# Kernel tuning notes

Measured on AMD Instinct MI355X. Metric: run time of the kernel, lower is better.

The kernel has to match this reference:

```python
import jax, jax.numpy as jnp
import numpy as np
import math

B, C, H, W = 32, 128, 32, 32
NUM_HEADS = 4
GROUPS = 32
EPS = 1e-5


def setup_inputs() -> dict:
    key = jax.random.key(0)
    ks = jax.random.split(key, 6)
    x = jax.random.normal(ks[0], (B, C, H, W), jnp.float32)
    norm_w = 1.0 + 0.1 * jax.random.normal(ks[1], (C,), jnp.float32)
    norm_b = 0.1 * jax.random.normal(ks[2], (C,), jnp.float32)
    qkv_w = jax.random.normal(ks[3], (3 * C, C), jnp.float32) / math.sqrt(C)
    proj_w = jax.random.normal(ks[4], (C, C), jnp.float32) / math.sqrt(C)
    proj_b = 0.01 * jax.random.normal(ks[5], (C,), jnp.float32)
    return {"x": x, "norm_w": norm_w, "norm_b": norm_b, "qkv_w": qkv_w,
            "proj_w": proj_w, "proj_b": proj_b}


def _group_norm(x, w, b):
    b_, c, h, w_ = x.shape
    xg = x.reshape(b_, GROUPS, c // GROUPS, h, w_)
    mu = xg.mean(axis=(2, 3, 4), keepdims=True)
    var = xg.var(axis=(2, 3, 4), keepdims=True)
    xn = ((xg - mu) * jax.lax.rsqrt(var + EPS)).reshape(b_, c, h, w_)
    return xn * w[None, :, None, None] + b[None, :, None, None]


def reference(x, norm_w, norm_b, qkv_w, proj_w, proj_b):
    b, c, h, w = x.shape
    nh = NUM_HEADS
    dh = c // nh
    hw = h * w
    xn = _group_norm(x, norm_w, norm_b)
    # 1x1 conv (no bias): [B,3C,H,W] flattened to [B,3C,HW]
    qkv = jnp.einsum('oc,bchw->bohw', qkv_w, xn).reshape(b, nh, 3 * dh, hw)
    # torch reshape (B*nh, 3C/nh, HW) + chunk(3, dim=1): per-head interleave
    q, k, v = qkv[:, :, :dh], qkv[:, :, dh:2 * dh], qkv[:, :, 2 * dh:]
    scale = 1.0 / math.sqrt(dh)
    # scale applied to BOTH q and k, as in the source
    attn = jnp.einsum('bhct,bhcs->bhts', q * scale, k * scale)  # [B,nh,HW,HW]
    attn = jax.nn.softmax(attn, axis=-1)
    hout = jnp.einsum('bhts,bhcs->bhct', attn, v).reshape(b, c, h, w)
    hout = jnp.einsum('oc,bchw->bohw', proj_w, hout) + proj_b[None, :, None, None]
    return hout + x
```

## Files before the change

### kernel.cpp

```cpp
#include <hip/hip_runtime.h>
#include <math.h>

#define BB 32
#define CC 128
#define HW 1024
#define NG 32
#define TPG 4096
#define QSZ ((size_t)BB * 4 * HW * 32)

typedef __attribute__((ext_vector_type(8))) short fragAB;
typedef __attribute__((ext_vector_type(4))) float fragC;
typedef __attribute__((ext_vector_type(8))) ushort ushort8v;

__device__ __forceinline__ ushort f2bf(float f) {
  union { float f; uint u; } v; v.f = f;
  uint r = v.u + 0x7FFFu + ((v.u >> 16) & 1u);
  return (ushort)(r >> 16);
}
__device__ __forceinline__ uint pack2(float lo, float hi) {
  return __builtin_amdgcn_perm(__float_as_uint(hi), __float_as_uint(lo), 0x07060302u);
}
__device__ __forceinline__ float bflo(uint u) { return __uint_as_float(u << 16); }
__device__ __forceinline__ float bfhi(uint u) { return __uint_as_float(u & 0xffff0000u); }
__device__ __forceinline__ int vswz(int row, int g) {
  return row * 128 + 16 * (g ^ (row & 7));
}

__global__ __launch_bounds__(256) void gn_stats(const float* __restrict__ x,
    float2* __restrict__ stats, const float* __restrict__ qkvw,
    const float* __restrict__ projw, ushort* __restrict__ wq16,
    ushort* __restrict__ wp16) {
  if (blockIdx.x >= 1024) {
    int idx = (blockIdx.x - 1024) * 256 + threadIdx.x;
    if (idx < 49152) wq16[idx] = f2bf(qkvw[idx]);
    else             wp16[idx - 49152] = f2bf(projw[idx - 49152]);
    return;
  }
  int blk = blockIdx.x;
  int b = blk >> 5, g = blk & 31;
  const float4* xp4 = (const float4*)(x + ((size_t)(b * CC + g * 4)) * HW);
  float s = 0.f, s2 = 0.f;
  #pragma unroll
  for (int i = 0; i < 4; ++i) {
    float4 v = xp4[threadIdx.x + i * 256];
    s  += v.x + v.y + v.z + v.w;
    s2 += v.x * v.x + v.y * v.y + v.z * v.z + v.w * v.w;
  }
  #pragma unroll
  for (int off = 32; off; off >>= 1) {
    s  += __shfl_down(s, off, 64);
    s2 += __shfl_down(s2, off, 64);
  }
  __shared__ float ls[4], ls2[4];
  int lane = threadIdx.x & 63, wid = threadIdx.x >> 6;
  if (lane == 0) { ls[wid] = s; ls2[wid] = s2; }
  __syncthreads();
  if (threadIdx.x == 0) {
    float a  = ls[0] + ls[1] + ls[2] + ls[3];
    float a2 = ls2[0] + ls2[1] + ls2[2] + ls2[3];
    float mu = a * (1.f / TPG);
    float var = a2 * (1.f / TPG) - mu * mu;
    stats[blk] = make_float2(mu, rsqrtf(var + 1e-5f));
  }
}

template<int PROJ>
__global__ __launch_bounds__(256) void mgemm(
    const ushort* __restrict__ W16, const ushort* __restrict__ X16,
    const float* __restrict__ xf, const float2* __restrict__ stats,
    const float* __restrict__ gw, const float* __restrict__ gb,
    ushort* __restrict__ Qb, float* __restrict__ out,
    const float* __restrict__ bias, const float* __restrict__ resid) {
  __shared__ ushort Xs[64 * 128];
  int b = blockIdx.z, t0 = blockIdx.x * 64;
  int tid = threadIdx.x;
  int lane = tid & 63, w = tid >> 6, lc = lane & 15, lg = lane >> 4;
  int wo = w >> 1, wt = w & 1;

  if constexpr (PROJ == 0) {
    int tq = tid & 15, co = tid >> 4;
    const float* xb = xf + (size_t)b * CC * HW + t0 + tq * 4;
    float wsc[8], bsc[8];
    {
      float2 s0 = stats[b * 32 + co * 2];
      float2 s1 = stats[b * 32 + co * 2 + 1];
      #pragma unroll
      for (int cc = 0; cc < 8; ++cc) {
        float rst = (cc < 4) ? s0.y : s1.y;
        float mu  = (cc < 4) ? s0.x : s1.x;
        float g = gw[co * 8 + cc];
        wsc[cc] = g * rst;
        bsc[cc] = gb[co * 8 + cc] - mu * wsc[cc];
      }
    }
    union { float4 v; float f[4]; } vv[8];
    #pragma unroll
    for (int cc = 0; cc < 8; ++cc)
      vv[cc].v = *(const float4*)&xb[(size_t)(co * 8 + cc) * HW];
    #pragma unroll
    for (int tt = 0; tt < 4; ++tt) {
      int row = tq * 4 + tt;
      ushort8v r;
      #pragma unroll
      for (int cc = 0; cc < 8; ++cc)
        r[cc] = f2bf(vv[cc].f[tt] * wsc[cc] + bsc[cc]);
      int byt = (row * 256 + co * 16) ^ ((row & 7) << 4);
      *(ushort8v*)((char*)Xs + byt) = r;
    }
  } else {
    const char* src = (const char*)(X16 + ((size_t)b * HW + t0) * CC);
    char* dst = (char*)Xs;
    #pragma unroll
    for (int it = 0; it < 4; ++it) {
      int flat = tid * 16 + it * 4096;
      uint4 v = *(const uint4*)(src + flat);
      *(uint4*)(dst + (flat ^ (((flat >> 8) & 7) << 4))) = v;
    }
  }
  __syncthreads();

  auto load_af = [&](fragAB af[2][4], int o0) {
    #pragma unroll
    for (int i = 0; i < 2; ++i)
      #pragma unroll
      for (int kc = 0; kc < 4; ++kc)
        af[i][kc] = *(const fragAB*)&W16[(size_t)(o0 + wo * 32 + i * 16 + lc) * 128 + kc * 32 + lg * 8];
  };

  auto kloop = [&](fragAB af[2][4], fragC acc[2][2]) {
    #pragma unroll
    for (int i = 0; i < 2; ++i)
      #pragma unroll
      for (int j = 0; j < 2; ++j)
        acc[i][j] = (fragC){0.f, 0.f, 0.f, 0.f};
    #pragma unroll
    for (int kc = 0; kc < 4; ++kc) {
      fragAB bf[2];
      #pragma unroll
      for (int j = 0; j < 2; ++j) {
        int row = wt * 32 + j * 16 + lc;
        int byt = (row * 256 + kc * 64 + lg * 16) ^ ((row & 7) << 4);
        bf[j] = *(const fragAB*)((const char*)Xs + byt);
      }
      #pragma unroll
      for (int i = 0; i < 2; ++i)
        #pragma unroll
        for (int j = 0; j < 2; ++j)
          acc[i][j] = __builtin_amdgcn_mfma_f32_16x16x32_bf16(af[i][kc], bf[j], acc[i][j], 0, 0, 0);
    }
  };

  if constexpr (PROJ == 0) {
    auto epi = [&](fragC acc[2][2], int o0) {
      #pragma unroll
      for (int i = 0; i < 2; ++i) {
        int ob = o0 + wo * 32 + i * 16;
        int blk = ob >> 5;
        int hh = blk / 3, kind = blk % 3;
        size_t bh = (size_t)b * 4 + hh;
        float sc = (kind == 0) ? (0.03125f * 1.44269504f) : 1.f;
        #pragma unroll
        for (int j = 0; j < 2; ++j) {
          if (kind < 2) {
            ushort* dst = (kind == 0) ? Qb : (Qb + QSZ);
            int s16 = (t0 >> 4) + wt * 2 + j;
            int eo = s16 * 512 + (((ob & 16) >> 3) + (lg >> 1)) * 128 + lc * 8 + (lg & 1) * 4;
            ushort4 rv;
            rv.x = f2bf(acc[i][j][0] * sc); rv.y = f2bf(acc[i][j][1] * sc);
            rv.z = f2bf(acc[i][j][2] * sc); rv.w = f2bf(acc[i][j][3] * sc);
            *(ushort4*)&dst[bh * 32768 + eo] = rv;
          } else {
            ushort* Vb = Qb + 2 * QSZ;
            int eo = (t0 >> 6) * 2048 + ((ob & 16) >> 4) * 1024
                   + (wt * 4 + j * 2 + (lc >> 3)) * 128 + (lc & 7);
            #pragma unroll
            for (int r = 0; r < 4; ++r)
              Vb[bh * 32768 + eo + (lg * 4 + r) * 8] = f2bf(acc[i][j][r]);
          }
        }
      }
    };

    int oy = blockIdx.y * 192;
    fragAB afA[2][4], afB[2][4];
    fragC acc[2][2];
    load_af(afA, oy);
    load_af(afB, oy + 64);
    kloop(afA, acc);
    epi(acc, oy);
    load_af(afA, oy + 128);
    kloop(afB, acc);
    epi(acc, oy + 64);
    kloop(afA, acc);
    epi(acc, oy + 128);
  } else {
    int o0 = blockIdx.y * 64;
    fragAB af[2][4];
    fragC acc[2][2];
    load_af(af, o0);
    kloop(af, acc);
    #pragma unroll
    for (int i = 0; i < 2; ++i)
      #pragma unroll
      for (int j = 0; j < 2; ++j) {
        int t = t0 + wt * 32 + j * 16 + lc;
        #pragma unroll
        for (int r = 0; r < 4; ++r) {
          int o = o0 + wo * 32 + i * 16 + lg * 4 + r;
          size_t idx = ((size_t)b * CC + o) * HW + t;
          out[idx] = acc[i][j][r] + bias[o] + resid[idx];
        }
      }
  }
}

__global__ __launch_bounds__(256) void attn7(
    const ushort* __restrict__ Qb, const ushort* __restrict__ Kb,
    const ushort* __restrict__ Vb, ushort* __restrict__ ao16) {
  __shared__ char arena[16384];

  int tid = threadIdx.x;
  int w = tid >> 6, lane = tid & 63, lc = lane & 15, lg = lane >> 4;
  int lb = blockIdx.x;
  int gp = (lb & 7) * 256 + (lb >> 3);
  int bh = gp >> 4, qp = gp & 15;
  int h = bh & 3, b = bh >> 2;
  int qt = qp * 2 + (w >> 1);
  int sh = w & 1;
  int t0 = qt * 32;

  const ushort* Qg = Qb + (size_t)bh * 32768 + (size_t)qt * 1024 + lane * 8;
  const ushort* Kg = Kb + (size_t)bh * 32768 + lane * 8;
  const ushort* Vg = Vb + (size_t)bh * 32768 + lane * 8;

  fragAB q0 = *(const fragAB*)&Qg[0];
  fragAB q1 = *(const fragAB*)&Qg[512];

  fragC a00 = {0.f,0.f,0.f,0.f}, a01 = {0.f,0.f,0.f,0.f};
  fragC a10 = {0.f,0.f,0.f,0.f}, a11 = {0.f,0.f,0.f,0.f};
  float l0 = 0.f, l1 = 0.f;
  char* wreg = arena + w * 4096;

  for (int i = sh * 8; i < sh * 8 + 8; ++i) {
    const ushort* Kt = Kg + i * 2048;
    const ushort* Vt = Vg + i * 2048;
    fragAB kf[4], vf[4];
    #pragma unroll
    for (int j = 0; j < 4; ++j) kf[j] = *(const fragAB*)&Kt[j * 512];
    #pragma unroll
    for (int u = 0; u < 4; ++u) vf[u] = *(const fragAB*)&Vt[u * 512];

    #pragma unroll
    for (int ts = 0; ts < 2; ++ts) {
      fragAB qf = ts ? q1 : q0;
      char* PsB = wreg + ts * 2048;
      fragC S[4];
      #pragma unroll
      for (int j = 0; j < 4; ++j) {
        fragC z = {0.f,0.f,0.f,0.f};
        S[j] = __builtin_amdgcn_mfma_f32_16x16x32_bf16(kf[j], qf, z, 0, 0, 0);
      }
      float rs = 0.f;
      #pragma unroll
      for (int j = 0; j < 4; ++j) {
        float p0 = __builtin_amdgcn_exp2f(S[j][0]), p1 = __builtin_amdgcn_exp2f(S[j][1]);
        float p2 = __builtin_amdgcn_exp2f(S[j][2]), p3 = __builtin_amdgcn_exp2f(S[j][3]);
        rs += (p0 + p1) + (p2 + p3);
        uint2 wv2;
        wv2.x = pack2(p0, p1);
        wv2.y = pack2(p2, p3);
        int g = j * 2 + (lg >> 1);
        *(uint2*)(PsB + lc * 128 + 16 * (g ^ (lc & 7)) + (lg & 1) * 8) = wv2;
      }
      if (ts) l1 += rs; else l0 += rs;
      fragC* aA = ts ? &a01 : &a00;
      fragC* aB = ts ? &a11 : &a10;
      fragAB bp0 = *(const fragAB*)(PsB + vswz(lc, lg));
      fragAB bp1 = *(const fragAB*)(PsB + vswz(lc, 4 + lg));
      *aA = __builtin_amdgcn_mfma_f32_16x16x32_bf16(vf[0], bp0, *aA, 0, 0, 0);
      *aA = __builtin_amdgcn_mfma_f32_16x16x32_bf16(vf[1], bp1, *aA, 0, 0, 0);
      *aB = __builtin_amdgcn_mfma_f32_16x16x32_bf16(vf[2], bp0, *aB, 0, 0, 0);
      *aB = __builtin_amdgcn_mfma_f32_16x16x32_bf16(vf[3], bp1, *aB, 0, 0, 0);
    }
  }

  if (sh == 1) {
    char* slot = wreg + lane * 40;
    uint2 u;
    u.x = pack2(a00[0], a00[1]); u.y = pack2(a00[2], a00[3]);
    *(uint2*)(slot) = u;
    u.x = pack2(a10[0], a10[1]); u.y = pack2(a10[2], a10[3]);
    *(uint2*)(slot + 8) = u;
    u.x = pack2(a01[0], a01[1]); u.y = pack2(a01[2], a01[3]);
    *(uint2*)(slot + 16) = u;
    u.x = pack2(a11[0], a11[1]); u.y = pack2(a11[2], a11[3]);
    *(uint2*)(slot + 24) = u;
    *(float2*)(slot + 32) = make_float2(l0, l1);
  }
  __syncthreads();
  if (sh == 1) return;

  {
    const char* slot = arena + (w + 1) * 4096 + lane * 40;
    uint2 u0 = *(const uint2*)(slot);
    uint2 u1 = *(const uint2*)(slot + 8);
    uint2 u2 = *(const uint2*)(slot + 16);
    uint2 u3 = *(const uint2*)(slot + 24);
    float2 lv = *(const float2*)(slot + 32);
    a00[0] += bflo(u0.x); a00[1] += bfhi(u0.x); a00[2] += bflo(u0.y); a00[3] += bfhi(u0.y);
    a10[0] += bflo(u1.x); a10[1] += bfhi(u1.x); a10[2] += bflo(u1.y); a10[3] += bfhi(u1.y);
    a01[0] += bflo(u2.x); a01[1] += bfhi(u2.x); a01[2] += bflo(u2.y); a01[3] += bfhi(u2.y);
    a11[0] += bflo(u3.x); a11[1] += bfhi(u3.x); a11[2] += bflo(u3.y); a11[3] += bfhi(u3.y);
    l0 += lv.x; l1 += lv.y;
  }

  l0 += __shfl_xor(l0, 16); l0 += __shfl_xor(l0, 32);
  l1 += __shfl_xor(l1, 16); l1 += __shfl_xor(l1, 32);
  float il0 = 1.f / l0, il1 = 1.f / l1;

  ushort* Ol = (ushort*)wreg;
  uint2 u;
  u.x = pack2(a00[0] * il0, a00[1] * il0); u.y = pack2(a00[2] * il0, a00[3] * il0);
  *(uint2*)&Ol[lc * 40 + lg * 4] = u;
  u.x = pack2(a10[0] * il0, a10[1] * il0); u.y = pack2(a10[2] * il0, a10[3] * il0);
  *(uint2*)&Ol[lc * 40 + 16 + lg * 4] = u;
  u.x = pack2(a01[0] * il1, a01[1] * il1); u.y = pack2(a01[2] * il1, a01[3] * il1);
  *(uint2*)&Ol[(lc + 16) * 40 + lg * 4] = u;
  u.x = pack2(a11[0] * il1, a11[1] * il1); u.y = pack2(a11[2] * il1, a11[3] * il1);
  *(uint2*)&Ol[(lc + 16) * 40 + 16 + lg * 4] = u;

  int row = lane >> 1, half = lane & 1;
  uint4 v0 = *(uint4*)&Ol[row * 40 + half * 16];
  uint4 v1 = *(uint4*)&Ol[row * 40 + half * 16 + 8];
  ushort* dst = &ao16[((size_t)b * HW + t0 + row) * CC + h * 32 + half * 16];
  *(uint4*)dst = v0;
  *(uint4*)(dst + 8) = v1;
}

extern "C" void kernel_launch(void* const* d_in, const int* in_sizes, int n_in,
                              void* d_out, int out_size, void* d_ws, size_t ws_size,
                              hipStream_t stream) {
  (void)in_sizes; (void)n_in; (void)out_size; (void)ws_size;
  const float* x     = (const float*)d_in[0];
  const float* gw    = (const float*)d_in[1];
  const float* gb    = (const float*)d_in[2];
  const float* qkvw  = (const float*)d_in[3];
  const float* projw = (const float*)d_in[4];
  const float* projb = (const float*)d_in[5];
  float* out = (float*)d_out;

  char* wsb = (char*)d_ws;
  ushort* ao16 = (ushort*)wsb;
  ushort* Qb   = (ushort*)(wsb + ((size_t)8 << 20));
  ushort* Kb   = Qb + QSZ;
  ushort* Vb   = Qb + 2 * QSZ;
  ushort* wq16 = (ushort*)(wsb + ((size_t)32 << 20));
  ushort* wp16 = (ushort*)(wsb + ((size_t)32 << 20) + (128 << 10));
  float2* stats = (float2*)(wsb + ((size_t)32 << 20) + (256 << 10));

  gn_stats<<<dim3(BB * NG + 256), 256, 0, stream>>>(x, stats, qkvw, projw, wq16, wp16);
  mgemm<0><<<dim3(16, 2, BB), 256, 0, stream>>>(wq16, nullptr, x, stats, gw, gb,
                                                Qb, nullptr, nullptr, nullptr);
  attn7<<<dim3(2048), 256, 0, stream>>>(Qb, Kb, Vb, ao16);
  mgemm<1><<<dim3(16, 2, BB), 256, 0, stream>>>(wp16, ao16, nullptr, nullptr, nullptr, nullptr,
                                                nullptr, out, projb, x);
}
```

Baseline: 66.01 us.

## Cache bf16 copy of x in stats pass, merge proj output tiles, unroll attention loop

The group-norm stats kernel now also writes a bf16 copy of x, and the QKV GEMM reads that copy instead of fp32 x, halving its input bytes. This costs an extra write in the stats kernel and applies normalization to bf16-rounded inputs, which adds some precision loss. The projection GEMM now computes both 64-row output halves in one block, halving its grid and reusing the staged activation tile. The attention K/V loop is unrolled by 2.

```diff
diff --git a/kernel.cpp b/kernel.cpp
--- a/kernel.cpp
+++ b/kernel.cpp
@@ -17,6 +17,9 @@
   uint r = v.u + 0x7FFFu + ((v.u >> 16) & 1u);
   return (ushort)(r >> 16);
 }
+__device__ __forceinline__ float bf2f(ushort u) {
+  return __uint_as_float((uint)u << 16);
+}
 __device__ __forceinline__ uint pack2(float lo, float hi) {
   return __builtin_amdgcn_perm(__float_as_uint(hi), __float_as_uint(lo), 0x07060302u);
 }
@@ -27,9 +30,9 @@
 }
 
 __global__ __launch_bounds__(256) void gn_stats(const float* __restrict__ x,
-    float2* __restrict__ stats, const float* __restrict__ qkvw,
-    const float* __restrict__ projw, ushort* __restrict__ wq16,
-    ushort* __restrict__ wp16) {
+    float2* __restrict__ stats, ushort* __restrict__ x16,
+    const float* __restrict__ qkvw, const float* __restrict__ projw,
+    ushort* __restrict__ wq16, ushort* __restrict__ wp16) {
   if (blockIdx.x >= 1024) {
     int idx = (blockIdx.x - 1024) * 256 + threadIdx.x;
     if (idx < 49152) wq16[idx] = f2bf(qkvw[idx]);
@@ -39,12 +42,17 @@
   int blk = blockIdx.x;
   int b = blk >> 5, g = blk & 31;
   const float4* xp4 = (const float4*)(x + ((size_t)(b * CC + g * 4)) * HW);
+  ushort* xo = x16 + ((size_t)(b * CC + g * 4)) * HW;
   float s = 0.f, s2 = 0.f;
   #pragma unroll
   for (int i = 0; i < 4; ++i) {
-    float4 v = xp4[threadIdx.x + i * 256];
+    int idx = threadIdx.x + i * 256;
+    float4 v = xp4[idx];
     s  += v.x + v.y + v.z + v.w;
     s2 += v.x * v.x + v.y * v.y + v.z * v.z + v.w * v.w;
+    ushort4 u;
+    u.x = f2bf(v.x); u.y = f2bf(v.y); u.z = f2bf(v.z); u.w = f2bf(v.w);
+    *(ushort4*)&xo[idx * 4] = u;
   }
   #pragma unroll
   for (int off = 32; off; off >>= 1) {
@@ -67,7 +75,7 @@
 template<int PROJ>
 __global__ __launch_bounds__(256) void mgemm(
     const ushort* __restrict__ W16, const ushort* __restrict__ X16,
-    const float* __restrict__ xf, const float2* __restrict__ stats,
+    const ushort* __restrict__ x16, const float2* __restrict__ stats,
     const float* __restrict__ gw, const float* __restrict__ gb,
     ushort* __restrict__ Qb, float* __restrict__ out,
     const float* __restrict__ bias, const float* __restrict__ resid) {
@@ -79,7 +87,7 @@
 
   if constexpr (PROJ == 0) {
     int tq = tid & 15, co = tid >> 4;
-    const float* xb = xf + (size_t)b * CC * HW + t0 + tq * 4;
+    const ushort* xb = x16 + (size_t)b * CC * HW + t0 + tq * 4;
     float wsc[8], bsc[8];
     {
       float2 s0 = stats[b * 32 + co * 2];
@@ -93,17 +101,19 @@
         bsc[cc] = gb[co * 8 + cc] - mu * wsc[cc];
       }
     }
-    union { float4 v; float f[4]; } vv[8];
+    ushort4 uv[8];
     #pragma unroll
     for (int cc = 0; cc < 8; ++cc)
-      vv[cc].v = *(const float4*)&xb[(size_t)(co * 8 + cc) * HW];
+      uv[cc] = *(const ushort4*)&xb[(size_t)(co * 8 + cc) * HW];
     #pragma unroll
     for (int tt = 0; tt < 4; ++tt) {
       int row = tq * 4 + tt;
       ushort8v r;
       #pragma unroll
-      for (int cc = 0; cc < 8; ++cc)
-        r[cc] = f2bf(vv[cc].f[tt] * wsc[cc] + bsc[cc]);
+      for (int cc = 0; cc < 8; ++cc) {
+        ushort e = (tt == 0) ? uv[cc].x : (tt == 1) ? uv[cc].y : (tt == 2) ? uv[cc].z : uv[cc].w;
+        r[cc] = f2bf(bf2f(e) * wsc[cc] + bsc[cc]);
+      }
       int byt = (row * 256 + co * 16) ^ ((row & 7) << 4);
       *(ushort8v*)((char*)Xs + byt) = r;
     }
@@ -194,23 +204,28 @@
     kloop(afA, acc);
     epi(acc, oy + 128);
   } else {
-    int o0 = blockIdx.y * 64;
-    fragAB af[2][4];
+    auto epi = [&](fragC acc[2][2], int o0) {
+      #pragma unroll
+      for (int i = 0; i < 2; ++i)
+        #pragma unroll
+        for (int j = 0; j < 2; ++j) {
+          int t = t0 + wt * 32 + j * 16 + lc;
+          #pragma unroll
+          for (int r = 0; r < 4; ++r) {
+            int o = o0 + wo * 32 + i * 16 + lg * 4 + r;
+            size_t idx = ((size_t)b * CC + o) * HW + t;
+            out[idx] = acc[i][j][r] + bias[o] + resid[idx];
+          }
+        }
+    };
+    fragAB afA[2][4], afB[2][4];
     fragC acc[2][2];
-    load_af(af, o0);
-    kloop(af, acc);
-    #pragma unroll
-    for (int i = 0; i < 2; ++i)
-      #pragma unroll
-      for (int j = 0; j < 2; ++j) {
-        int t = t0 + wt * 32 + j * 16 + lc;
-        #pragma unroll
-        for (int r = 0; r < 4; ++r) {
-          int o = o0 + wo * 32 + i * 16 + lg * 4 + r;
-          size_t idx = ((size_t)b * CC + o) * HW + t;
-          out[idx] = acc[i][j][r] + bias[o] + resid[idx];
-        }
-      }
+    load_af(afA, 0);
+    load_af(afB, 64);
+    kloop(afA, acc);
+    epi(acc, 0);
+    kloop(afB, acc);
+    epi(acc, 64);
   }
 }
 
@@ -241,6 +256,7 @@
   float l0 = 0.f, l1 = 0.f;
   char* wreg = arena + w * 4096;
 
+  #pragma unroll 2
   for (int i = sh * 8; i < sh * 8 + 8; ++i) {
     const ushort* Kt = Kg + i * 2048;
     const ushort* Vt = Vg + i * 2048;
@@ -357,11 +373,12 @@
   ushort* wq16 = (ushort*)(wsb + ((size_t)32 << 20));
   ushort* wp16 = (ushort*)(wsb + ((size_t)32 << 20) + (128 << 10));
   float2* stats = (float2*)(wsb + ((size_t)32 << 20) + (256 << 10));
-
-  gn_stats<<<dim3(BB * NG + 256), 256, 0, stream>>>(x, stats, qkvw, projw, wq16, wp16);
-  mgemm<0><<<dim3(16, 2, BB), 256, 0, stream>>>(wq16, nullptr, x, stats, gw, gb,
+  ushort* x16  = (ushort*)(wsb + ((size_t)34 << 20));
+
+  gn_stats<<<dim3(BB * NG + 256), 256, 0, stream>>>(x, stats, x16, qkvw, projw, wq16, wp16);
+  mgemm<0><<<dim3(16, 2, BB), 256, 0, stream>>>(wq16, nullptr, x16, stats, gw, gb,
                                                 Qb, nullptr, nullptr, nullptr);
   attn7<<<dim3(2048), 256, 0, stream>>>(Qb, Kb, Vb, ao16);
-  mgemm<1><<<dim3(16, 2, BB), 256, 0, stream>>>(wp16, ao16, nullptr, nullptr, nullptr, nullptr,
+  mgemm<1><<<dim3(16, 1, BB), 256, 0, stream>>>(wp16, ao16, nullptr, nullptr, nullptr, nullptr,
                                                 nullptr, out, projb, x);
 }
```

New measurement: 67.32 us. Within noise of the previous version (+2.0%).
